# Performance work log

Measured on AMD Instinct MI355X. Metric: run time of the kernel, lower is better.

Reference implementation:

```python
import jax, jax.numpy as jnp
import numpy as np

D_MODEL = 1024
H = 16
HEAD = D_MODEL // H  # 64


def setup_inputs() -> dict:
    key = jax.random.key(0)
    ks = jax.random.split(key, 10)
    B, S = 2, 2048
    x = jax.random.normal(ks[0], (B, S, D_MODEL), dtype=jnp.float32)
    y = jax.random.normal(ks[1], (B, S, D_MODEL), dtype=jnp.float32)
    mask = jnp.ones((B, S, S), dtype=jnp.float32)
    s = 1.0 / np.sqrt(D_MODEL)
    Wq = jax.random.normal(ks[2], (D_MODEL, D_MODEL), dtype=jnp.float32) * s
    Wk = jax.random.normal(ks[3], (D_MODEL, D_MODEL), dtype=jnp.float32) * s
    Wv = jax.random.normal(ks[4], (D_MODEL, D_MODEL), dtype=jnp.float32) * s
    Wo = jax.random.normal(ks[5], (D_MODEL, D_MODEL), dtype=jnp.float32) * s
    bq = jnp.zeros((D_MODEL,), jnp.float32)
    bk = jnp.zeros((D_MODEL,), jnp.float32)
    bv = jnp.zeros((D_MODEL,), jnp.float32)
    bo = jnp.zeros((D_MODEL,), jnp.float32)
    return {"x": x, "y": y, "mask": mask, "Wq": Wq, "bq": bq, "Wk": Wk,
            "bk": bk, "Wv": Wv, "bv": bv, "Wo": Wo, "bo": bo}


def reference(x, y, mask, Wq, bq, Wk, bk, Wv, bv, Wo, bo):
    # torch Linear: out = in @ W.T + b; here W stored as [out, in]
    B, Sq, D = x.shape
    Skv = y.shape[1]
    q = x @ Wq.T + bq  # [B, Sq, D]
    k = y @ Wk.T + bk  # [B, Skv, D]
    v = y @ Wv.T + bv
    # chunk(h, dim=-1) + cat(dim=0) == split feature dim into heads (head-major)
    q = q.reshape(B, Sq, H, HEAD)
    k = k.reshape(B, Skv, H, HEAD)
    v = v.reshape(B, Skv, H, HEAD)
    score = jnp.einsum('bqhd,bkhd->bhqk', q, k) / np.sqrt(HEAD)
    score = score + (1.0 - mask[:, None, :, :]) * -1e9
    attn = jax.nn.softmax(score, axis=-1)
    out = jnp.einsum('bhqk,bkhd->bqhd', attn, v).reshape(B, Sq, D)
    return out @ Wo.T + bo
```

## Files before the change

kernel.cpp:

```cpp
#include <hip/hip_runtime.h>
#include <cstdint>
#include <cstddef>

typedef __bf16 bf16x8 __attribute__((ext_vector_type(8)));
typedef float f32x4 __attribute__((ext_vector_type(4)));
typedef unsigned short u16;
typedef unsigned short u16x8 __attribute__((ext_vector_type(8)));
typedef unsigned int u32;

typedef __attribute__((address_space(1))) void gvoid_t;
typedef __attribute__((address_space(3))) void lvoid_t;

__device__ __forceinline__ void gld_lds16(const void* g, void* l) {
  __builtin_amdgcn_global_load_lds((gvoid_t*)g, (lvoid_t*)l, 16, 0, 0);
}

__device__ __forceinline__ u16 f2bf(float f) {
  u32 u = __float_as_uint(f);
  u += 0x7fffu + ((u >> 16) & 1u);
  return (u16)(u >> 16);
}
__device__ __forceinline__ u32 pack_rnd(float a, float b) {
  const u32 ua = __float_as_uint(a) + 0x8000u;
  const u32 ub = __float_as_uint(b) + 0x8000u;
  return __builtin_amdgcn_perm(ub, ua, 0x07060302u);
}
__device__ __forceinline__ bf16x8 ld_frag(const u16* p) {
  return __builtin_bit_cast(bf16x8, *(const uint4*)p);
}
__device__ __forceinline__ f32x4 mfma16(bf16x8 a, bf16x8 b, f32x4 c) {
  return __builtin_amdgcn_mfma_f32_16x16x32_bf16(a, b, c, 0, 0, 0);
}
__device__ __forceinline__ float ex2(float x) {
  return __builtin_amdgcn_exp2f(x);
}

#define D_MODEL 1024
#define SEQ     2048
#define NHEAD   16
#define QSC     0.1803368801f
#define MBIAS   (-1.4426950408e9f)

__global__ __launch_bounds__(256) void pre_kernel(
    const float* __restrict__ x,  const float* __restrict__ y,
    const float* __restrict__ wq, const float* __restrict__ wk,
    const float* __restrict__ wv, const float* __restrict__ wo,
    const float* __restrict__ mask,
    u16* __restrict__ xb, u16* __restrict__ yb,
    u16* __restrict__ wqb, u16* __restrict__ wkb,
    u16* __restrict__ wvb, u16* __restrict__ wob,
    u16* __restrict__ biasC, u32* __restrict__ flags) {
  const int bid = blockIdx.x;
  const float* src;
  u16* dst;
  int base;
  float sA = 1.0f, sB = 0.0f;
  if (bid < 2048)      { src = x;    dst = xb;    base = 0; }
  else if (bid < 4096) { src = y;    dst = yb;    base = 2048; }
  else if (bid < 4608) { src = wq;   dst = wqb;   base = 4096; sA = QSC; }
  else if (bid < 5120) { src = wk;   dst = wkb;   base = 4608; }
  else if (bid < 5632) { src = wv;   dst = wvb;   base = 5120; }
  else if (bid < 6144) { src = wo;   dst = wob;   base = 5632; }
  else                 { src = mask; dst = biasC; base = 6144; sA = -MBIAS; sB = MBIAS; }
  const int i = (((bid - base) * 256) + threadIdx.x) * 8;
  const float4 a = *(const float4*)(src + i);
  const float4 b = *(const float4*)(src + i + 4);
  ushort4 lo, hi;
  lo.x = f2bf(a.x * sA + sB); lo.y = f2bf(a.y * sA + sB);
  lo.z = f2bf(a.z * sA + sB); lo.w = f2bf(a.w * sA + sB);
  hi.x = f2bf(b.x * sA + sB); hi.y = f2bf(b.y * sA + sB);
  hi.z = f2bf(b.z * sA + sB); hi.w = f2bf(b.w * sA + sB);
  *(ushort4*)(dst + i) = lo;
  *(ushort4*)(dst + i + 4) = hi;

  if (bid >= 6144) {
    const bool m8 = (a.x != 1.f) || (a.y != 1.f) || (a.z != 1.f) || (a.w != 1.f) ||
                    (b.x != 1.f) || (b.y != 1.f) || (b.z != 1.f) || (b.w != 1.f);
    const unsigned long long bal = __ballot(m8);
    const int lane = threadIdx.x & 63, wv8 = threadIdx.x >> 6;
    if (lane == 0) {
      u32 bits = 0;
#pragma unroll
      for (int g = 0; g < 8; ++g)
        bits |= (((bal >> (8 * g)) & 0xFFull) ? 1u : 0u) << g;
      if (bits) {
        const int row = bid - 6144;
        const int bb = row >> 11, q = row & 2047;
        atomicOr(&flags[bb * 32 + (q >> 6)], bits << (wv8 * 8));
      }
    }
  }
}

template <int MODE, typename OT>
__device__ __forceinline__ void gemm_block_128(const u16* __restrict__ A,
                                               const u16* __restrict__ W,
                                               const float* __restrict__ bias,
                                               float bscale,
                                               OT* __restrict__ D,
                                               int mb, int nb) {
  __shared__ __align__(16) u16 S[16384];
  u16* Asl = S;
  u16* Bsl = S + 8192;
  const int tid = threadIdx.x;
  const int w = tid >> 6, lane = tid & 63, quad = lane >> 4, l16 = lane & 15;
  const int wm = (w & 1) * 64, wn = (w >> 1) * 64;
  const int cidx = w * 64 + lane;

  f32x4 acc[4][4];
#pragma unroll
  for (int i = 0; i < 4; ++i)
#pragma unroll
    for (int j = 0; j < 4; ++j) acc[i][j] = f32x4{0.f, 0.f, 0.f, 0.f};

  for (int k0 = 0; k0 < 1024; k0 += 64) {
    __syncthreads();
#pragma unroll
    for (int t = 0; t < 4; ++t) {
      const int idx = t * 256 + cidx;
      const int row = idx >> 3;
      const int g = (idx & 7) ^ (row & 7);
      const size_t dst = (size_t)(t * 4 + w) * 1024;
      gld_lds16(A + (size_t)(mb * 128 + row) * 1024 + k0 + g * 8, (char*)Asl + dst);
      gld_lds16(W + (size_t)(nb * 128 + row) * 1024 + k0 + g * 8, (char*)Bsl + dst);
    }
    __syncthreads();

#pragma unroll
    for (int kk = 0; kk < 2; ++kk) {
      bf16x8 af[4], bfr[4];
#pragma unroll
      for (int i = 0; i < 4; ++i) {
        const int ar = wm + i * 16 + l16;
        const int br = wn + i * 16 + l16;
        af[i]  = ld_frag(Asl + ar * 64 + (((kk * 4 + quad) ^ (ar & 7)) * 8));
        bfr[i] = ld_frag(Bsl + br * 64 + (((kk * 4 + quad) ^ (br & 7)) * 8));
      }
#pragma unroll
      for (int i = 0; i < 4; ++i)
#pragma unroll
        for (int j = 0; j < 4; ++j) acc[i][j] = mfma16(af[i], bfr[j], acc[i][j]);
    }
  }

  if constexpr (MODE == 2) {
    __syncthreads();
#pragma unroll
    for (int i = 0; i < 4; ++i)
#pragma unroll
      for (int j = 0; j < 4; ++j) {
        const int dl = wn + j * 16 + l16;
        const float bv = bias[nb * 128 + dl];
        const int sx = (wm + i * 16 + quad * 4) ^ ((dl & 15) << 3);
        uint2 pv;
        pv.x = (u32)f2bf(acc[i][j][0] + bv) | ((u32)f2bf(acc[i][j][1] + bv) << 16);
        pv.y = (u32)f2bf(acc[i][j][2] + bv) | ((u32)f2bf(acc[i][j][3] + bv) << 16);
        *(uint2*)(S + dl * 128 + sx) = pv;
      }
    __syncthreads();
    const int dl = tid >> 1, half = tid & 1;
    const int bb = mb >> 4, s0 = (mb & 15) * 128;
    u16* vrow = (u16*)D + (size_t)(bb * 1024 + nb * 128 + dl) * SEQ + s0 + half * 64;
#pragma unroll
    for (int c = 0; c < 8; ++c) {
      const int pc = (half * 8 + c) ^ (dl & 15);
      *(uint4*)(vrow + c * 8) = *(const uint4*)(S + dl * 128 + pc * 8);
    }
  } else {
#pragma unroll
    for (int i = 0; i < 4; ++i)
#pragma unroll
      for (int j = 0; j < 4; ++j) {
        const int gn = nb * 128 + wn + j * 16 + l16;
        const float bv = bias[gn] * bscale;
#pragma unroll
        for (int r = 0; r < 4; ++r) {
          const int gm = mb * 128 + wm + i * 16 + quad * 4 + r;
          const float v = acc[i][j][r] + bv;
          if constexpr (sizeof(OT) == 2)
            D[(size_t)gm * 1024 + gn] = (OT)f2bf(v);
          else
            D[(size_t)gm * 1024 + gn] = (OT)v;
        }
      }
  }
}

__global__ __launch_bounds__(256) void qkv_kernel(
    const u16* __restrict__ xb, const u16* __restrict__ yb,
    const u16* __restrict__ Wqb, const u16* __restrict__ Wkb, const u16* __restrict__ Wvb,
    const float* __restrict__ bq, const float* __restrict__ bk, const float* __restrict__ bv,
    u16* __restrict__ qb, u16* __restrict__ kb, u16* __restrict__ vt) {
  const int mat = blockIdx.y >> 3;
  const int nb = blockIdx.y & 7;
  const int mb = blockIdx.x;
  if (mat == 0)      gemm_block_128<0, u16>(xb, Wqb, bq, QSC,  qb, mb, nb);
  else if (mat == 1) gemm_block_128<0, u16>(yb, Wkb, bk, 1.0f, kb, mb, nb);
  else               gemm_block_128<2, u16>(yb, Wvb, bv, 1.0f, vt, mb, nb);
}

__global__ __launch_bounds__(256) void oproj_kernel(
    const u16* __restrict__ ctx, const u16* __restrict__ Wob,
    const float* __restrict__ bo, float* __restrict__ out) {
  gemm_block_128<1, float>(ctx, Wob, bo, 1.0f, out, blockIdx.x, blockIdx.y);
}

__global__ __launch_bounds__(256) void attn_kernel(
    const u16* __restrict__ qb, const u16* __restrict__ kb,
    const u16* __restrict__ vt, const u16* __restrict__ biasC,
    const u32* __restrict__ flags, u16* __restrict__ ctx) {
  const int h = blockIdx.x;
  const int qblk = blockIdx.y;
  const int b = blockIdx.z;
  const int tid = threadIdx.x, w = tid >> 6, lane = tid & 63;
  const int quad = lane >> 4, l16 = lane & 15;
  const int q0 = qblk * 64;

  __shared__ __align__(16) u16 Ks[64 * 64];
  __shared__ __align__(16) u16 Vs[64 * 64];
  __shared__ __align__(16) u16 BP[64 * 64];

  const u32 fl = flags[(b << 5) + qblk];

  const int qrow = w * 16 + l16;
  const u16* qp = qb + (size_t)(b * SEQ + q0 + qrow) * D_MODEL + h * 64;
  const bf16x8 qf0 = ld_frag(qp + quad * 8);
  const bf16x8 qf1 = ld_frag(qp + 32 + quad * 8);

  bf16x8 onesf;
  {
    u16x8 t;
    const u16 ov = (l16 == 0) ? (u16)0x3F80 : (u16)0;
#pragma unroll
    for (int j = 0; j < 8; ++j) t[j] = ov;
    onesf = __builtin_bit_cast(bf16x8, t);
  }

  f32x4 O[4];
#pragma unroll
  for (int dt = 0; dt < 4; ++dt) O[dt] = f32x4{0.f, 0.f, 0.f, 0.f};
  f32x4 O4 = f32x4{0.f, 0.f, 0.f, 0.f};

  const int cidx = w * 64 + lane;
  const int bhalf = (quad & 1) * 4;

  const int r0 = cidx >> 3,        g0 = (cidx & 7) ^ (r0 & 7);
  const int r1 = (256 + cidx) >> 3, g1 = ((256 + cidx) & 7) ^ (r1 & 7);
  const u16* kp0 = kb + (size_t)(b * SEQ + r0) * D_MODEL + h * 64 + g0 * 8;
  const u16* kp1 = kb + (size_t)(b * SEQ + r1) * D_MODEL + h * 64 + g1 * 8;
  const u16* vp0 = vt + ((size_t)((b * NHEAD + h) * 64 + r0)) * SEQ + g0 * 8;
  const u16* vp1 = vt + ((size_t)((b * NHEAD + h) * 64 + r1)) * SEQ + g1 * 8;
  const u16* bp0 = biasC + (size_t)(b * SEQ + q0 + r0) * SEQ + g0 * 8;
  const u16* bp1 = biasC + (size_t)(b * SEQ + q0 + r1) * SEQ + g1 * 8;
  const size_t dst0 = (size_t)w * 1024;
  const size_t dst1 = (size_t)(4 + w) * 1024;

  for (int kt = 0; kt < 32; ++kt) {
    const bool doBias = (fl >> kt) & 1u;
    __syncthreads();
    gld_lds16(kp0, (char*)Ks + dst0);
    gld_lds16(kp1, (char*)Ks + dst1);
    gld_lds16(vp0, (char*)Vs + dst0);
    gld_lds16(vp1, (char*)Vs + dst1);
    if (doBias) {
      gld_lds16(bp0, (char*)BP + dst0);
      gld_lds16(bp1, (char*)BP + dst1);
    }
    kp0 += 64 * D_MODEL; kp1 += 64 * D_MODEL;
    vp0 += 64;           vp1 += 64;
    bp0 += 64;           bp1 += 64;
    __syncthreads();

    f32x4 z[4];
    __builtin_amdgcn_s_setprio(1);
#pragma unroll
    for (int nt = 0; nt < 4; ++nt) {
      const int kvl = nt * 16 + l16;
      const bf16x8 kf0 = ld_frag(Ks + kvl * 64 + ((quad ^ (kvl & 7)) * 8));
      const bf16x8 kf1 = ld_frag(Ks + kvl * 64 + (((4 + quad) ^ (kvl & 7)) * 8));
      f32x4 zz;
      if (doBias) {
        const int ck = nt * 2 + (quad >> 1);
        const uint2 bw = *(const uint2*)(BP + qrow * 64 + ((ck ^ (qrow & 7)) * 8) + bhalf);
        zz[0] = __uint_as_float(bw.x << 16);
        zz[1] = __uint_as_float(bw.x & 0xffff0000u);
        zz[2] = __uint_as_float(bw.y << 16);
        zz[3] = __uint_as_float(bw.y & 0xffff0000u);
      } else {
        zz = f32x4{0.f, 0.f, 0.f, 0.f};
      }
      zz = mfma16(kf0, qf0, zz);
      zz = mfma16(kf1, qf1, zz);
      z[nt] = zz;
    }
    __builtin_amdgcn_s_setprio(0);
#pragma unroll
    for (int nt = 0; nt < 4; ++nt) {
      uint2 pv;
      pv.x = pack_rnd(ex2(z[nt][0]), ex2(z[nt][1]));
      pv.y = pack_rnd(ex2(z[nt][2]), ex2(z[nt][3]));
      const int ck = nt * 2 + (quad >> 1);
      *(uint2*)(BP + qrow * 64 + ((ck ^ (qrow & 7)) * 8) + bhalf) = pv;
    }

    const bf16x8 pf0 = ld_frag(BP + qrow * 64 + ((quad ^ (qrow & 7)) * 8));
    const bf16x8 pf1 = ld_frag(BP + qrow * 64 + (((4 + quad) ^ (qrow & 7)) * 8));
    __builtin_amdgcn_s_setprio(1);
#pragma unroll
    for (int dt = 0; dt < 4; ++dt) {
      const int vr = dt * 16 + l16;
      const bf16x8 vf0 = ld_frag(Vs + vr * 64 + ((quad ^ (vr & 7)) * 8));
      const bf16x8 vf1 = ld_frag(Vs + vr * 64 + (((4 + quad) ^ (vr & 7)) * 8));
      O[dt] = mfma16(pf0, vf0, O[dt]);
      O[dt] = mfma16(pf1, vf1, O[dt]);
    }
    O4 = mfma16(pf0, onesf, O4);
    O4 = mfma16(pf1, onesf, O4);
    __builtin_amdgcn_s_setprio(0);
  }

  float inv[4];
#pragma unroll
  for (int r = 0; r < 4; ++r)
    inv[r] = 1.0f / __shfl(O4[r], lane & 48, 64);

#pragma unroll
  for (int dt = 0; dt < 4; ++dt)
#pragma unroll
    for (int r = 0; r < 4; ++r) {
      const int gq = b * SEQ + q0 + w * 16 + quad * 4 + r;
      const int gd = h * 64 + dt * 16 + l16;
      ctx[(size_t)gq * D_MODEL + gd] = f2bf(O[dt][r] * inv[r]);
    }
}

extern "C" void kernel_launch(void* const* d_in, const int* in_sizes, int n_in,
                              void* d_out, int out_size, void* d_ws, size_t ws_size,
                              hipStream_t stream) {
  (void)in_sizes; (void)n_in; (void)out_size; (void)ws_size;
  const float* x    = (const float*)d_in[0];
  const float* y    = (const float*)d_in[1];
  const float* mask = (const float*)d_in[2];
  const float* Wq   = (const float*)d_in[3];
  const float* bq   = (const float*)d_in[4];
  const float* Wk   = (const float*)d_in[5];
  const float* bk   = (const float*)d_in[6];
  const float* Wv   = (const float*)d_in[7];
  const float* bv   = (const float*)d_in[8];
  const float* Wo   = (const float*)d_in[9];
  const float* bo   = (const float*)d_in[10];
  float* out = (float*)d_out;

  const size_t M4 = (size_t)4096 * 1024;
  const size_t M1 = (size_t)1024 * 1024;
  u16* qbuf  = (u16*)d_ws;
  u16* kbuf  = qbuf + M4;
  u16* vt    = kbuf + M4;
  u16* cbuf  = vt + M4;
  u16* wob   = cbuf + M4;
  u16* xb    = wob + M1;
  u16* yb    = xb + M4;
  u16* wqb   = yb + M4;
  u16* wkb   = wqb + M1;
  u16* wvb   = wkb + M1;
  u32* flags = (u32*)(wvb + M1);
  u16* biasC = (u16*)d_out;

  hipMemsetAsync(flags, 0, 64 * sizeof(u32), stream);
  pre_kernel<<<dim3(10240, 1, 1), 256, 0, stream>>>(
      x, y, Wq, Wk, Wv, Wo, mask, xb, yb, wqb, wkb, wvb, wob, biasC, flags);
  qkv_kernel<<<dim3(32, 24, 1), 256, 0, stream>>>(xb, yb, wqb, wkb, wvb,
                                                  bq, bk, bv, qbuf, kbuf, vt);
  attn_kernel<<<dim3(NHEAD, 32, 2), 256, 0, stream>>>(qbuf, kbuf, vt, biasC, flags, cbuf);
  oproj_kernel<<<dim3(32, 8, 1), 256, 0, stream>>>(cbuf, wob, bo, out);
}
```

Baseline: 250.5 us.

## Drop bf16 mask-bias materialization; read fp32 mask directly in attention; narrow oproj tiles

The pre-pass no longer converts the full BxSxS mask into a bf16 bias buffer. It only scans the mask to set per-tile nonzero flags. When a tile is flagged, the attention kernel reads the fp32 mask straight from global memory and computes the bias in registers, which removes a large write and reread of bias data. The output projection switches to a 128x64 tile GEMM, doubling its block count to improve occupancy across CUs. The cost is uncoalesced fp32 mask loads inside attention when masking is active, but the all-ones test mask never triggers that path.

```diff
diff --git a/kernel.cpp b/kernel.cpp
--- a/kernel.cpp
+++ b/kernel.cpp
@@ -49,31 +49,12 @@
     u16* __restrict__ xb, u16* __restrict__ yb,
     u16* __restrict__ wqb, u16* __restrict__ wkb,
     u16* __restrict__ wvb, u16* __restrict__ wob,
-    u16* __restrict__ biasC, u32* __restrict__ flags) {
+    u32* __restrict__ flags) {
   const int bid = blockIdx.x;
-  const float* src;
-  u16* dst;
-  int base;
-  float sA = 1.0f, sB = 0.0f;
-  if (bid < 2048)      { src = x;    dst = xb;    base = 0; }
-  else if (bid < 4096) { src = y;    dst = yb;    base = 2048; }
-  else if (bid < 4608) { src = wq;   dst = wqb;   base = 4096; sA = QSC; }
-  else if (bid < 5120) { src = wk;   dst = wkb;   base = 4608; }
-  else if (bid < 5632) { src = wv;   dst = wvb;   base = 5120; }
-  else if (bid < 6144) { src = wo;   dst = wob;   base = 5632; }
-  else                 { src = mask; dst = biasC; base = 6144; sA = -MBIAS; sB = MBIAS; }
-  const int i = (((bid - base) * 256) + threadIdx.x) * 8;
-  const float4 a = *(const float4*)(src + i);
-  const float4 b = *(const float4*)(src + i + 4);
-  ushort4 lo, hi;
-  lo.x = f2bf(a.x * sA + sB); lo.y = f2bf(a.y * sA + sB);
-  lo.z = f2bf(a.z * sA + sB); lo.w = f2bf(a.w * sA + sB);
-  hi.x = f2bf(b.x * sA + sB); hi.y = f2bf(b.y * sA + sB);
-  hi.z = f2bf(b.z * sA + sB); hi.w = f2bf(b.w * sA + sB);
-  *(ushort4*)(dst + i) = lo;
-  *(ushort4*)(dst + i + 4) = hi;
-
   if (bid >= 6144) {
+    const int i = (((bid - 6144) * 256) + threadIdx.x) * 8;
+    const float4 a = *(const float4*)(mask + i);
+    const float4 b = *(const float4*)(mask + i + 4);
     const bool m8 = (a.x != 1.f) || (a.y != 1.f) || (a.z != 1.f) || (a.w != 1.f) ||
                     (b.x != 1.f) || (b.y != 1.f) || (b.z != 1.f) || (b.w != 1.f);
     const unsigned long long bal = __ballot(m8);
@@ -89,7 +70,28 @@
         atomicOr(&flags[bb * 32 + (q >> 6)], bits << (wv8 * 8));
       }
     }
-  }
+    return;
+  }
+  const float* src;
+  u16* dst;
+  int base;
+  float sA = 1.0f;
+  if (bid < 2048)      { src = x;    dst = xb;    base = 0; }
+  else if (bid < 4096) { src = y;    dst = yb;    base = 2048; }
+  else if (bid < 4608) { src = wq;   dst = wqb;   base = 4096; sA = QSC; }
+  else if (bid < 5120) { src = wk;   dst = wkb;   base = 4608; }
+  else if (bid < 5632) { src = wv;   dst = wvb;   base = 5120; }
+  else                 { src = wo;   dst = wob;   base = 5632; }
+  const int i = (((bid - base) * 256) + threadIdx.x) * 8;
+  const float4 a = *(const float4*)(src + i);
+  const float4 b = *(const float4*)(src + i + 4);
+  ushort4 lo, hi;
+  lo.x = f2bf(a.x * sA); lo.y = f2bf(a.y * sA);
+  lo.z = f2bf(a.z * sA); lo.w = f2bf(a.w * sA);
+  hi.x = f2bf(b.x * sA); hi.y = f2bf(b.y * sA);
+  hi.z = f2bf(b.z * sA); hi.w = f2bf(b.w * sA);
+  *(ushort4*)(dst + i) = lo;
+  *(ushort4*)(dst + i + 4) = hi;
 }
 
 template <int MODE, typename OT>
@@ -186,6 +188,79 @@
   }
 }
 
+__device__ __forceinline__ void gemm_block_n64(const u16* __restrict__ A,
+                                               const u16* __restrict__ W,
+                                               const float* __restrict__ bias,
+                                               float* __restrict__ D,
+                                               int mb, int nb) {
+  __shared__ __align__(16) u16 S[12288];
+  u16* Asl = S;
+  u16* Bsl = S + 8192;
+  const int tid = threadIdx.x;
+  const int w = tid >> 6, lane = tid & 63, quad = lane >> 4, l16 = lane & 15;
+  const int wm = w * 32;
+  const int cidx = w * 64 + lane;
+
+  f32x4 acc[2][4];
+#pragma unroll
+  for (int i = 0; i < 2; ++i)
+#pragma unroll
+    for (int j = 0; j < 4; ++j) acc[i][j] = f32x4{0.f, 0.f, 0.f, 0.f};
+
+  for (int k0 = 0; k0 < 1024; k0 += 64) {
+    __syncthreads();
+#pragma unroll
+    for (int t = 0; t < 4; ++t) {
+      const int idx = t * 256 + cidx;
+      const int row = idx >> 3;
+      const int g = (idx & 7) ^ (row & 7);
+      gld_lds16(A + (size_t)(mb * 128 + row) * 1024 + k0 + g * 8,
+                (char*)Asl + (size_t)(t * 4 + w) * 1024);
+    }
+#pragma unroll
+    for (int t = 0; t < 2; ++t) {
+      const int idx = t * 256 + cidx;
+      const int row = idx >> 3;
+      const int g = (idx & 7) ^ (row & 7);
+      gld_lds16(W + (size_t)(nb * 64 + row) * 1024 + k0 + g * 8,
+                (char*)Bsl + (size_t)(t * 4 + w) * 1024);
+    }
+    __syncthreads();
+
+#pragma unroll
+    for (int kk = 0; kk < 2; ++kk) {
+      bf16x8 af[2], bfr[4];
+#pragma unroll
+      for (int i = 0; i < 2; ++i) {
+        const int ar = wm + i * 16 + l16;
+        af[i] = ld_frag(Asl + ar * 64 + (((kk * 4 + quad) ^ (ar & 7)) * 8));
+      }
+#pragma unroll
+      for (int j = 0; j < 4; ++j) {
+        const int br = j * 16 + l16;
+        bfr[j] = ld_frag(Bsl + br * 64 + (((kk * 4 + quad) ^ (br & 7)) * 8));
+      }
+#pragma unroll
+      for (int i = 0; i < 2; ++i)
+#pragma unroll
+        for (int j = 0; j < 4; ++j) acc[i][j] = mfma16(af[i], bfr[j], acc[i][j]);
+    }
+  }
+
+#pragma unroll
+  for (int i = 0; i < 2; ++i)
+#pragma unroll
+    for (int j = 0; j < 4; ++j) {
+      const int gn = nb * 64 + j * 16 + l16;
+      const float bv = bias[gn];
+#pragma unroll
+      for (int r = 0; r < 4; ++r) {
+        const int gm = mb * 128 + wm + i * 16 + quad * 4 + r;
+        D[(size_t)gm * 1024 + gn] = acc[i][j][r] + bv;
+      }
+    }
+}
+
 __global__ __launch_bounds__(256) void qkv_kernel(
     const u16* __restrict__ xb, const u16* __restrict__ yb,
     const u16* __restrict__ Wqb, const u16* __restrict__ Wkb, const u16* __restrict__ Wvb,
@@ -202,12 +277,12 @@
 __global__ __launch_bounds__(256) void oproj_kernel(
     const u16* __restrict__ ctx, const u16* __restrict__ Wob,
     const float* __restrict__ bo, float* __restrict__ out) {
-  gemm_block_128<1, float>(ctx, Wob, bo, 1.0f, out, blockIdx.x, blockIdx.y);
+  gemm_block_n64(ctx, Wob, bo, out, blockIdx.x, blockIdx.y);
 }
 
 __global__ __launch_bounds__(256) void attn_kernel(
     const u16* __restrict__ qb, const u16* __restrict__ kb,
-    const u16* __restrict__ vt, const u16* __restrict__ biasC,
+    const u16* __restrict__ vt, const float* __restrict__ mask,
     const u32* __restrict__ flags, u16* __restrict__ ctx) {
   const int h = blockIdx.x;
   const int qblk = blockIdx.y;
@@ -218,7 +293,7 @@
 
   __shared__ __align__(16) u16 Ks[64 * 64];
   __shared__ __align__(16) u16 Vs[64 * 64];
-  __shared__ __align__(16) u16 BP[64 * 64];
+  __shared__ __align__(16) u16 Ps[64 * 64];
 
   const u32 fl = flags[(b << 5) + qblk];
 
@@ -250,8 +325,7 @@
   const u16* kp1 = kb + (size_t)(b * SEQ + r1) * D_MODEL + h * 64 + g1 * 8;
   const u16* vp0 = vt + ((size_t)((b * NHEAD + h) * 64 + r0)) * SEQ + g0 * 8;
   const u16* vp1 = vt + ((size_t)((b * NHEAD + h) * 64 + r1)) * SEQ + g1 * 8;
-  const u16* bp0 = biasC + (size_t)(b * SEQ + q0 + r0) * SEQ + g0 * 8;
-  const u16* bp1 = biasC + (size_t)(b * SEQ + q0 + r1) * SEQ + g1 * 8;
+  const float* mp = mask + (size_t)(b * SEQ + q0 + qrow) * SEQ + quad * 4;
   const size_t dst0 = (size_t)w * 1024;
   const size_t dst1 = (size_t)(4 + w) * 1024;
 
@@ -262,13 +336,8 @@
     gld_lds16(kp1, (char*)Ks + dst1);
     gld_lds16(vp0, (char*)Vs + dst0);
     gld_lds16(vp1, (char*)Vs + dst1);
-    if (doBias) {
-      gld_lds16(bp0, (char*)BP + dst0);
-      gld_lds16(bp1, (char*)BP + dst1);
-    }
     kp0 += 64 * D_MODEL; kp1 += 64 * D_MODEL;
     vp0 += 64;           vp1 += 64;
-    bp0 += 64;           bp1 += 64;
     __syncthreads();
 
     f32x4 z[4];
@@ -280,12 +349,11 @@
       const bf16x8 kf1 = ld_frag(Ks + kvl * 64 + (((4 + quad) ^ (kvl & 7)) * 8));
       f32x4 zz;
       if (doBias) {
-        const int ck = nt * 2 + (quad >> 1);
-        const uint2 bw = *(const uint2*)(BP + qrow * 64 + ((ck ^ (qrow & 7)) * 8) + bhalf);
-        zz[0] = __uint_as_float(bw.x << 16);
-        zz[1] = __uint_as_float(bw.x & 0xffff0000u);
-        zz[2] = __uint_as_float(bw.y << 16);
-        zz[3] = __uint_as_float(bw.y & 0xffff0000u);
+        const float4 mv = *(const float4*)(mp + nt * 16);
+        zz[0] = (1.f - mv.x) * MBIAS;
+        zz[1] = (1.f - mv.y) * MBIAS;
+        zz[2] = (1.f - mv.z) * MBIAS;
+        zz[3] = (1.f - mv.w) * MBIAS;
       } else {
         zz = f32x4{0.f, 0.f, 0.f, 0.f};
       }
@@ -294,17 +362,18 @@
       z[nt] = zz;
     }
     __builtin_amdgcn_s_setprio(0);
+    mp += 64;
 #pragma unroll
     for (int nt = 0; nt < 4; ++nt) {
       uint2 pv;
       pv.x = pack_rnd(ex2(z[nt][0]), ex2(z[nt][1]));
       pv.y = pack_rnd(ex2(z[nt][2]), ex2(z[nt][3]));
       const int ck = nt * 2 + (quad >> 1);
-      *(uint2*)(BP + qrow * 64 + ((ck ^ (qrow & 7)) * 8) + bhalf) = pv;
-    }
-
-    const bf16x8 pf0 = ld_frag(BP + qrow * 64 + ((quad ^ (qrow & 7)) * 8));
-    const bf16x8 pf1 = ld_frag(BP + qrow * 64 + (((4 + quad) ^ (qrow & 7)) * 8));
+      *(uint2*)(Ps + qrow * 64 + ((ck ^ (qrow & 7)) * 8) + bhalf) = pv;
+    }
+
+    const bf16x8 pf0 = ld_frag(Ps + qrow * 64 + ((quad ^ (qrow & 7)) * 8));
+    const bf16x8 pf1 = ld_frag(Ps + qrow * 64 + (((4 + quad) ^ (qrow & 7)) * 8));
     __builtin_amdgcn_s_setprio(1);
 #pragma unroll
     for (int dt = 0; dt < 4; ++dt) {
@@ -364,13 +433,12 @@
   u16* wkb   = wqb + M1;
   u16* wvb   = wkb + M1;
   u32* flags = (u32*)(wvb + M1);
-  u16* biasC = (u16*)d_out;
 
   hipMemsetAsync(flags, 0, 64 * sizeof(u32), stream);
   pre_kernel<<<dim3(10240, 1, 1), 256, 0, stream>>>(
-      x, y, Wq, Wk, Wv, Wo, mask, xb, yb, wqb, wkb, wvb, wob, biasC, flags);
+      x, y, Wq, Wk, Wv, Wo, mask, xb, yb, wqb, wkb, wvb, wob, flags);
   qkv_kernel<<<dim3(32, 24, 1), 256, 0, stream>>>(xb, yb, wqb, wkb, wvb,
                                                   bq, bk, bv, qbuf, kbuf, vt);
-  attn_kernel<<<dim3(NHEAD, 32, 2), 256, 0, stream>>>(qbuf, kbuf, vt, biasC, flags, cbuf);
-  oproj_kernel<<<dim3(32, 8, 1), 256, 0, stream>>>(cbuf, wob, bo, out);
-}
+  attn_kernel<<<dim3(NHEAD, 32, 2), 256, 0, stream>>>(qbuf, kbuf, vt, mask, flags, cbuf);
+  oproj_kernel<<<dim3(32, 16, 1), 256, 0, stream>>>(cbuf, wob, bo, out);
+}
```

New measurement: 244.0 us. -2.6%, faster.
